# Optimization experiments

Hardware: AMD Instinct MI355X
Metric: run time of the kernel (lower is better)

## Reference

```python
import jax, jax.numpy as jnp
import numpy as np

EMB = 1024
HEADS = 16
DH = EMB // HEADS
EPS = 1e-5


def setup_inputs() -> dict:
    key = jax.random.key(0)
    ks = jax.random.split(key, 8)
    s = 0.02
    return {
        "x": jax.random.normal(ks[0], (4, 2048, EMB), dtype=jnp.float32),
        "Wq": jax.random.normal(ks[1], (EMB, EMB), dtype=jnp.float32) * s,
        "Wk": jax.random.normal(ks[2], (EMB, EMB), dtype=jnp.float32) * s,
        "Wv": jax.random.normal(ks[3], (EMB, EMB), dtype=jnp.float32) * s,
        "Wo": jax.random.normal(ks[4], (EMB, EMB), dtype=jnp.float32) * s,
        "bo": jnp.zeros((EMB,), dtype=jnp.float32),
        "W1": jax.random.normal(ks[5], (EMB, 4 * EMB), dtype=jnp.float32) * s,
        "b1": jnp.zeros((4 * EMB,), dtype=jnp.float32),
        "W2": jax.random.normal(ks[6], (4 * EMB, EMB), dtype=jnp.float32) * s,
        "b2": jnp.zeros((EMB,), dtype=jnp.float32),
        "g1": jnp.ones((EMB,), dtype=jnp.float32),
        "beta1": jnp.zeros((EMB,), dtype=jnp.float32),
        "g2": jnp.ones((EMB,), dtype=jnp.float32),
        "beta2": jnp.zeros((EMB,), dtype=jnp.float32),
    }


def _layernorm(x, scale, bias):
    mean = jnp.mean(x, axis=-1, keepdims=True)
    var = jnp.mean((x - mean) ** 2, axis=-1, keepdims=True)  # unbiased=False
    return scale * ((x - mean) / jnp.sqrt(var + EPS)) + bias


def _attention(x, Wq, Wk, Wv, Wo, bo):
    B, S, _ = x.shape
    q = (x @ Wq).reshape(B, S, HEADS, DH).transpose(0, 2, 1, 3)  # b h s d
    k = (x @ Wk).reshape(B, S, HEADS, DH).transpose(0, 2, 1, 3)
    v = (x @ Wv).reshape(B, S, HEADS, DH).transpose(0, 2, 1, 3)
    scores = jnp.einsum("bhqd,bhkd->bhqk", q, k)
    causal = jnp.tril(jnp.ones((S, S), dtype=bool))
    scores = jnp.where(causal, scores, -jnp.inf)
    w = jax.nn.softmax(scores / jnp.sqrt(jnp.float32(DH)), axis=-1)
    ctx = jnp.einsum("bhqk,bhkd->bhqd", w, v).transpose(0, 2, 1, 3).reshape(B, S, HEADS * DH)
    return ctx @ Wo + bo


def reference(x, Wq, Wk, Wv, Wo, bo, W1, b1, W2, b2, g1, beta1, g2, beta2):
    # pre-LN attention + residual
    h = x + _attention(_layernorm(x, g1, beta1), Wq, Wk, Wv, Wo, bo)
    # pre-LN FFN (exact GELU, as torch nn.GELU default) + residual
    y = _layernorm(h, g2, beta2)
    y = jax.nn.gelu(y @ W1 + b1, approximate=False) @ W2 + b2
    return h + y
```

## Files before the change

### kernel.cpp

```cpp
#include <hip/hip_runtime.h>
#include <hip/hip_bf16.h>

#define EMB 1024
#define SEQ 2048
#define BATCH 4
#define TOK (BATCH*SEQ)
#define NH 16
#define DH 64
#define FF 4096

typedef unsigned short u16;
typedef __bf16 bf16x8 __attribute__((ext_vector_type(8)));
typedef float f32x4 __attribute__((ext_vector_type(4)));

union frag_u { uint4 u4; bf16x8 bf; u16 us[8]; };

__device__ __forceinline__ u16 f2bf(float f) {
  union { float f; unsigned u; } a; a.f = f;
  unsigned r = a.u + 0x7fffu + ((a.u >> 16) & 1u);
  return (u16)(r >> 16);
}
__device__ __forceinline__ float bf2f(u16 u) {
  union { unsigned u; float f; } a; a.u = ((unsigned)u) << 16; return a.f;
}
__device__ __forceinline__ unsigned cvt_pk_bf16(float lo, float hi) {
  unsigned r;
  asm("v_cvt_pk_bf16_f32 %0, %1, %2" : "=v"(r) : "v"(lo), "v"(hi));
  return r;
}
__device__ __forceinline__ float exp2_hw(float x) {
  float r;
  asm("v_exp_f32 %0, %1" : "=v"(r) : "v"(x));
  return r;
}

__device__ __forceinline__ void glds16(const void* g, void* l) {
  __builtin_amdgcn_global_load_lds((const __attribute__((address_space(1))) void*)g,
                                   (__attribute__((address_space(3))) void*)l, 16, 0, 0);
}

__device__ __forceinline__ float gelu_fast(float u) {
  float u2 = u * u;
  float c = fmaf(u2, 0.0356774081f, 0.7978845608f);
  float e = __expf(2.f * u * c);
  return u * e * __builtin_amdgcn_rcpf(e + 1.f);
}

__device__ __forceinline__ void cvt_t_body(const float* __restrict__ src,
                                           u16* __restrict__ dst,
                                           int N, int ldk, int bx, int by) {
  __shared__ float tile[32][33];
  int c0 = bx * 32, r0 = by * 32;
  int tc = threadIdx.x & 31, tr = threadIdx.x >> 5;
  #pragma unroll
  for (int p = 0; p < 4; p++)
    tile[tr + p * 8][tc] = src[(size_t)(r0 + tr + p * 8) * N + c0 + tc];
  __syncthreads();
  #pragma unroll
  for (int p = 0; p < 4; p++)
    dst[(size_t)(c0 + tr + p * 8) * ldk + r0 + tc] = f2bf(tile[tc][tr + p * 8]);
}

__global__ __launch_bounds__(256) void prep_kernel(const float* Wq, const float* Wk,
                                                   const float* Wv, const float* Wo,
                                                   const float* W1, const float* W2,
                                                   u16* wqkv_t, u16* wo_t,
                                                   u16* w1_t, u16* w2_t) {
  int id = blockIdx.x;
  if (id < 4096) {
    const float* s = (id < 1024) ? Wq : (id < 2048) ? Wk : (id < 3072) ? Wv : Wo;
    u16* d = (id < 1024) ? wqkv_t : (id < 2048) ? wqkv_t + 1024 * 1024
           : (id < 3072) ? wqkv_t + 2 * 1024 * 1024 : wo_t;
    int local = id & 1023;
    cvt_t_body(s, d, 1024, 1024, local & 31, local >> 5);
  } else if (id < 8192) {
    int local = id - 4096;
    cvt_t_body(W1, w1_t, 4096, 1024, local & 127, local >> 7);
  } else {
    int local = id - 8192;
    cvt_t_body(W2, w2_t, 1024, 4096, local & 31, local >> 5);
  }
}

template <int IN_BF16>
__global__ __launch_bounds__(256) void ln_kernel(const void* __restrict__ xv,
                                                 const float* __restrict__ g,
                                                 const float* __restrict__ be,
                                                 u16* __restrict__ out) {
  int wave = threadIdx.x >> 6, lane = threadIdx.x & 63;
  int row = blockIdx.x * 4 + wave;
  float v[16];
  float s = 0.f;
  if (IN_BF16) {
    const u16* xr = (const u16*)xv + (size_t)row * EMB;
    #pragma unroll
    for (int i = 0; i < 4; i++) {
      ushort4 u = *(const ushort4*)(xr + i * 256 + lane * 4);
      v[i * 4 + 0] = bf2f(u.x); v[i * 4 + 1] = bf2f(u.y);
      v[i * 4 + 2] = bf2f(u.z); v[i * 4 + 3] = bf2f(u.w);
      s += v[i * 4] + v[i * 4 + 1] + v[i * 4 + 2] + v[i * 4 + 3];
    }
  } else {
    const float* xr = (const float*)xv + (size_t)row * EMB;
    #pragma unroll
    for (int i = 0; i < 4; i++) {
      float4 u = *(const float4*)(xr + i * 256 + lane * 4);
      v[i * 4 + 0] = u.x; v[i * 4 + 1] = u.y; v[i * 4 + 2] = u.z; v[i * 4 + 3] = u.w;
      s += u.x + u.y + u.z + u.w;
    }
  }
  #pragma unroll
  for (int m = 1; m < 64; m <<= 1) s += __shfl_xor(s, m, 64);
  float mean = s * (1.f / EMB);
  float vs = 0.f;
  #pragma unroll
  for (int i = 0; i < 16; i++) { float dx = v[i] - mean; vs += dx * dx; }
  #pragma unroll
  for (int m = 1; m < 64; m <<= 1) vs += __shfl_xor(vs, m, 64);
  float inv = rsqrtf(vs * (1.f / EMB) + 1e-5f);
  u16* orow = out + (size_t)row * EMB;
  #pragma unroll
  for (int i = 0; i < 4; i++) {
    int c = i * 256 + lane * 4;
    float4 gv = *(const float4*)(g + c);
    float4 bv = *(const float4*)(be + c);
    ushort4 o;
    o.x = f2bf(gv.x * (v[i * 4 + 0] - mean) * inv + bv.x);
    o.y = f2bf(gv.y * (v[i * 4 + 1] - mean) * inv + bv.y);
    o.z = f2bf(gv.z * (v[i * 4 + 2] - mean) * inv + bv.z);
    o.w = f2bf(gv.w * (v[i * 4 + 3] - mean) * inv + bv.w);
    *(ushort4*)(orow + c) = o;
  }
}

template <int MODE>
__global__ __launch_bounds__(512) void gemm256(const u16* __restrict__ A,
                                               const u16* __restrict__ Bt,
                                               const float* __restrict__ bias,
                                               void* __restrict__ outp,
                                               int N, int K) {
  __shared__ __align__(16) u16 As[256 * 64];
  __shared__ __align__(16) u16 Bs[128 * 64];
  const int t = threadIdx.x;
  const int w = t >> 6, lane = t & 63;
  const int l15 = lane & 15, quad = lane >> 4;
  const int wr = w >> 1, wc = w & 1;

  const int gx = gridDim.x;
  const int nwg = gx * gridDim.y;
  const int id0 = blockIdx.y * gx + blockIdx.x;
  const int nid = (id0 & 7) * (nwg >> 3) + (id0 >> 3);
  const int rowBase = (nid / gx) * 256, colBase = (nid % gx) * 128;

  const int sr = lane >> 3;
  const int sc = ((lane & 7) ^ sr) * 8;
  const u16* gA = A + (size_t)(rowBase + w * 8 + sr) * K + sc;
  const u16* gB = Bt + (size_t)(colBase + w * 8 + sr) * K + sc;
  u16* lA = As + w * 8 * 64;
  u16* lB = Bs + w * 8 * 64;

  const int swz0 = (quad ^ (l15 & 7)) * 8;
  const int swz1 = ((quad + 4) ^ (l15 & 7)) * 8;

  f32x4 zero = {0.f, 0.f, 0.f, 0.f};
  f32x4 acc[4][4];
  #pragma unroll
  for (int i = 0; i < 4; i++)
    #pragma unroll
    for (int j = 0; j < 4; j++) acc[i][j] = zero;

  for (int k0 = 0; k0 < K; k0 += 64) {
    __syncthreads();
    #pragma unroll
    for (int j = 0; j < 4; j++)
      glds16(gA + (size_t)(j * 64) * K + k0, lA + j * 64 * 64);
    #pragma unroll
    for (int j = 0; j < 2; j++)
      glds16(gB + (size_t)(j * 64) * K + k0, lB + j * 64 * 64);
    __syncthreads();
    #pragma unroll
    for (int kk = 0; kk < 2; kk++) {
      const int so = kk ? swz1 : swz0;
      frag_u a4[4], b4[4];
      #pragma unroll
      for (int mi = 0; mi < 4; mi++)
        a4[mi].u4 = *(const uint4*)(As + (wr * 64 + mi * 16 + l15) * 64 + so);
      #pragma unroll
      for (int ni = 0; ni < 4; ni++)
        b4[ni].u4 = *(const uint4*)(Bs + (wc * 64 + ni * 16 + l15) * 64 + so);
      #pragma unroll
      for (int mi = 0; mi < 4; mi++)
        #pragma unroll
        for (int ni = 0; ni < 4; ni++)
          acc[mi][ni] = __builtin_amdgcn_mfma_f32_16x16x32_bf16(a4[mi].bf, b4[ni].bf, acc[mi][ni], 0, 0, 0);
    }
  }

  #pragma unroll
  for (int mi = 0; mi < 4; mi++) {
    #pragma unroll
    for (int ni = 0; ni < 4; ni++) {
      int col = colBase + wc * 64 + ni * 16 + l15;
      int row0 = rowBase + wr * 64 + mi * 16 + quad * 4;
      if (MODE == 1) {
        int mat = col >> 10, cc = col & 1023;
        int hh = cc >> 6, d = cc & 63;
        int b = row0 >> 11, s0 = row0 & 2047;
        if (mat == 2) {
          uint2 pk;
          pk.x = (unsigned)f2bf(acc[mi][ni][0]) | ((unsigned)f2bf(acc[mi][ni][1]) << 16);
          pk.y = (unsigned)f2bf(acc[mi][ni][2]) | ((unsigned)f2bf(acc[mi][ni][3]) << 16);
          *(uint2*)((u16*)outp + 2 * (size_t)TOK * EMB +
                    ((size_t)((b * NH + hh) * DH + d)) * SEQ + s0) = pk;
        } else {
          const float m = (mat == 0) ? 0.1803368801f : 1.f;
          #pragma unroll
          for (int r = 0; r < 4; r++)
            ((u16*)outp)[(size_t)mat * (TOK * EMB) +
                         (((size_t)(b * NH + hh) * SEQ + s0 + r) << 6) + d] = f2bf(acc[mi][ni][r] * m);
        }
      } else {
        #pragma unroll
        for (int r = 0; r < 4; r++) {
          float vv = gelu_fast(acc[mi][ni][r] + bias[col]);
          ((u16*)outp)[(size_t)(row0 + r) * N + col] = f2bf(vv);
        }
      }
    }
  }
}

template <int MODE>
__global__ __launch_bounds__(256) void gemm128(const u16* __restrict__ A,
                                               const u16* __restrict__ Bt,
                                               const float* __restrict__ bias,
                                               const void* __restrict__ resid,
                                               void* __restrict__ outp,
                                               int N, int K) {
  __shared__ __align__(16) u16 As[2][128 * 64];
  __shared__ __align__(16) u16 Bs[2][128 * 64];
  const int t = threadIdx.x;
  const int w = t >> 6, lane = t & 63;
  const int l15 = lane & 15, quad = lane >> 4;
  const int wr = w >> 1, wc = w & 1;

  const int gx = gridDim.x;
  const int nwg = gx * gridDim.y;
  const int id0 = blockIdx.y * gx + blockIdx.x;
  const int nid = (id0 & 7) * (nwg >> 3) + (id0 >> 3);
  const int rowBase = (nid / gx) * 128, colBase = (nid % gx) * 128;

  const int sr = lane >> 3;
  const int sc = ((lane & 7) ^ sr) * 8;
  const u16* gA = A + (size_t)(rowBase + w * 8 + sr) * K + sc;
  const u16* gB = Bt + (size_t)(colBase + w * 8 + sr) * K + sc;
  const int ldsOff = (w * 8) * 64;

  const int swz0 = (quad ^ (l15 & 7)) * 8;
  const int swz1 = ((quad + 4) ^ (l15 & 7)) * 8;

  f32x4 zero = {0.f, 0.f, 0.f, 0.f};
  f32x4 acc[4][4];
  #pragma unroll
  for (int i = 0; i < 4; i++)
    #pragma unroll
    for (int j = 0; j < 4; j++) acc[i][j] = zero;

  const int nt = K >> 6;
  #pragma unroll
  for (int j = 0; j < 4; j++) {
    glds16(gA + (size_t)(j * 32) * K, As[0] + ldsOff + j * 32 * 64);
    glds16(gB + (size_t)(j * 32) * K, Bs[0] + ldsOff + j * 32 * 64);
  }
  #pragma unroll
  for (int j = 0; j < 4; j++) {
    glds16(gA + (size_t)(j * 32) * K + 64, As[1] + ldsOff + j * 32 * 64);
    glds16(gB + (size_t)(j * 32) * K + 64, Bs[1] + ldsOff + j * 32 * 64);
  }

  for (int tt = 0; tt < nt; tt++) {
    const int cur = tt & 1;
    if (tt + 1 < nt) asm volatile("s_waitcnt vmcnt(8)" ::: "memory");
    else             asm volatile("s_waitcnt vmcnt(0)" ::: "memory");
    __builtin_amdgcn_sched_barrier(0);
    __builtin_amdgcn_s_barrier();

    const u16* as = As[cur];
    const u16* bs = Bs[cur];
    #pragma unroll
    for (int kk = 0; kk < 2; kk++) {
      const int so = kk ? swz1 : swz0;
      frag_u a4[4], b4[4];
      #pragma unroll
      for (int mi = 0; mi < 4; mi++)
        a4[mi].u4 = *(const uint4*)(as + (wr * 64 + mi * 16 + l15) * 64 + so);
      #pragma unroll
      for (int ni = 0; ni < 4; ni++)
        b4[ni].u4 = *(const uint4*)(bs + (wc * 64 + ni * 16 + l15) * 64 + so);
      #pragma unroll
      for (int mi = 0; mi < 4; mi++)
        #pragma unroll
        for (int ni = 0; ni < 4; ni++)
          acc[mi][ni] = __builtin_amdgcn_mfma_f32_16x16x32_bf16(a4[mi].bf, b4[ni].bf, acc[mi][ni], 0, 0, 0);
    }
    asm volatile("s_waitcnt lgkmcnt(0)" ::: "memory");
    __builtin_amdgcn_sched_barrier(0);
    __builtin_amdgcn_s_barrier();

    if (tt + 2 < nt) {
      const int k0 = (tt + 2) << 6;
      #pragma unroll
      for (int j = 0; j < 4; j++) {
        glds16(gA + (size_t)(j * 32) * K + k0, As[cur] + ldsOff + j * 32 * 64);
        glds16(gB + (size_t)(j * 32) * K + k0, Bs[cur] + ldsOff + j * 32 * 64);
      }
    }
  }

  #pragma unroll
  for (int mi = 0; mi < 4; mi++) {
    #pragma unroll
    for (int ni = 0; ni < 4; ni++) {
      int col = colBase + wc * 64 + ni * 16 + l15;
      int row0 = rowBase + wr * 64 + mi * 16 + quad * 4;
      #pragma unroll
      for (int r = 0; r < 4; r++) {
        int row = row0 + r;
        float vv = acc[mi][ni][r] + bias[col];
        if (MODE == 3) {
          vv += ((const float*)resid)[(size_t)row * N + col];
          ((u16*)outp)[(size_t)row * N + col] = f2bf(vv);
        } else {
          vv += bf2f(((const u16*)resid)[(size_t)row * N + col]);
          ((float*)outp)[(size_t)row * N + col] = vv;
        }
      }
    }
  }
}

__global__ __launch_bounds__(256) void attn_kernel(const u16* __restrict__ q,
                                                   const u16* __restrict__ k,
                                                   const u16* __restrict__ vt,
                                                   u16* __restrict__ ctx) {
  __shared__ __align__(16) u16 Ks[64 * 64];
  __shared__ __align__(16) u16 Vs[64 * 64];
  __shared__ __align__(16) u16 Ps[128 * 64];
  __shared__ float Ls[128];
  const int t = threadIdx.x;
  const int w = t >> 6, lane = t & 63;
  const int l15 = lane & 15, quad = lane >> 4;
  const int bh = blockIdx.x;
  const int qt = 15 - (int)blockIdx.y;
  const size_t base = (size_t)bh * SEQ * DH;
  const int bq = bh >> 4, hh = bh & 15;
  const int qBase = qt * 128;
  const int ktEnd = 2 * qt + 1;
  const int l7 = l15 & 7;

  const int r0 = w * 16 + (lane >> 3);
  const int scg = lane & 7;
  const int swzs = (scg ^ (r0 & 7)) * 8;
  const u16* gK = k + base + (size_t)r0 * DH + scg * 8;
  const u16* gV = vt + base + (size_t)r0 * SEQ + scg * 8;
  u16* sK0 = Ks + r0 * 64 + swzs;
  u16* sK1 = Ks + (r0 + 8) * 64 + swzs;
  u16* sV0 = Vs + r0 * 64 + swzs;
  u16* sV1 = Vs + (r0 + 8) * 64 + swzs;

  frag_u qf[2][2];
  #pragma unroll
  for (int ni = 0; ni < 2; ni++)
    #pragma unroll
    for (int ks = 0; ks < 2; ks++)
      qf[ni][ks].u4 = *(const uint4*)(q + base +
          (size_t)(qBase + w * 32 + ni * 16 + l15) * DH + ks * 32 + quad * 8);

  f32x4 zero = {0.f, 0.f, 0.f, 0.f};
  f32x4 oacc[2][4];
  #pragma unroll
  for (int mi = 0; mi < 2; mi++)
    #pragma unroll
    for (int n0 = 0; n0 < 4; n0++) oacc[mi][n0] = zero;
  float l0 = 0.f, l1 = 0.f;

  uint4 rK0 = *(const uint4*)(gK);
  uint4 rK1 = *(const uint4*)(gK + 8 * DH);
  uint4 rV0 = *(const uint4*)(gV);
  uint4 rV1 = *(const uint4*)(gV + (size_t)8 * SEQ);

  for (int kt = 0; kt <= ktEnd; kt++) {
    __syncthreads();
    *(uint4*)sK0 = rK0; *(uint4*)sK1 = rK1;
    *(uint4*)sV0 = rV0; *(uint4*)sV1 = rV1;
    __syncthreads();
    if (kt < ktEnd) {
      const int no = (kt + 1) * 64;
      rK0 = *(const uint4*)(gK + (size_t)no * DH);
      rK1 = *(const uint4*)(gK + (size_t)(no + 8) * DH);
      rV0 = *(const uint4*)(gV + no);
      rV1 = *(const uint4*)(gV + (size_t)8 * SEQ + no);
    }
    const int rel = kt - 2 * qt;
    if (rel == 1 && w < 2) continue;

    frag_u kf[4][2];
    #pragma unroll
    for (int mi = 0; mi < 4; mi++)
      #pragma unroll
      for (int ks = 0; ks < 2; ks++)
        kf[mi][ks].u4 = *(const uint4*)(Ks + (mi * 16 + l15) * 64 + (((ks * 4 + quad) ^ l7) * 8));
    f32x4 st[4][2];
    #pragma unroll
    for (int mi = 0; mi < 4; mi++)
      #pragma unroll
      for (int ni = 0; ni < 2; ni++) st[mi][ni] = zero;
    __builtin_amdgcn_s_setprio(1);
    #pragma unroll
    for (int ks = 0; ks < 2; ks++)
      #pragma unroll
      for (int mi = 0; mi < 4; mi++)
        #pragma unroll
        for (int ni = 0; ni < 2; ni++)
          st[mi][ni] = __builtin_amdgcn_mfma_f32_16x16x32_bf16(kf[mi][ks].bf, qf[ni][ks].bf, st[mi][ni], 0, 0, 0);
    __builtin_amdgcn_s_setprio(0);

    const bool doMask = (rel == 0 && w < 2) || (rel == 1);
    #pragma unroll
    for (int ni = 0; ni < 2; ni++) {
      const int qrow = qBase + w * 32 + ni * 16 + l15;
      float sum = 0.f;
      u16* prow = Ps + (w * 32 + ni * 16 + l15) * 64;
      #pragma unroll
      for (int mi = 0; mi < 4; mi++) {
        float p[4];
        if (doMask) {
          #pragma unroll
          for (int r = 0; r < 4; r++) {
            p[r] = exp2_hw(st[mi][ni][r]);
            if ((kt * 64 + mi * 16 + quad * 4 + r) > qrow) p[r] = 0.f;
            sum += p[r];
          }
        } else {
          #pragma unroll
          for (int r = 0; r < 4; r++) {
            p[r] = exp2_hw(st[mi][ni][r]);
            sum += p[r];
          }
        }
        uint2 pk;
        pk.x = cvt_pk_bf16(p[0], p[1]);
        pk.y = cvt_pk_bf16(p[2], p[3]);
        *(uint2*)(prow + (((mi * 2 + (quad >> 1)) ^ l7) * 8) + (quad & 1) * 4) = pk;
      }
      sum += __shfl_xor(sum, 16, 64);
      sum += __shfl_xor(sum, 32, 64);
      if (ni == 0) l0 += sum; else l1 += sum;
    }

    frag_u pa[2][2];
    #pragma unroll
    for (int mi = 0; mi < 2; mi++)
      #pragma unroll
      for (int ks = 0; ks < 2; ks++)
        pa[mi][ks].u4 = *(const uint4*)(Ps + (w * 32 + mi * 16 + l15) * 64 + (((ks * 4 + quad) ^ l7) * 8));
    __builtin_amdgcn_s_setprio(1);
    #pragma unroll
    for (int ks = 0; ks < 2; ks++)
      #pragma unroll
      for (int n0 = 0; n0 < 4; n0++) {
        frag_u b;
        b.u4 = *(const uint4*)(Vs + (n0 * 16 + l15) * 64 + (((ks * 4 + quad) ^ l7) * 8));
        #pragma unroll
        for (int mi = 0; mi < 2; mi++)
          oacc[mi][n0] = __builtin_amdgcn_mfma_f32_16x16x32_bf16(pa[mi][ks].bf, b.bf, oacc[mi][n0], 0, 0, 0);
      }
    __builtin_amdgcn_s_setprio(0);
  }

  if (quad == 0) {
    Ls[w * 32 + l15] = l0;
    Ls[w * 32 + 16 + l15] = l1;
  }
  #pragma unroll
  for (int mi = 0; mi < 2; mi++) {
    float il[4];
    #pragma unroll
    for (int r = 0; r < 4; r++) il[r] = 1.f / Ls[w * 32 + mi * 16 + quad * 4 + r];
    #pragma unroll
    for (int n0 = 0; n0 < 4; n0++) {
      int s = qBase + w * 32 + mi * 16 + quad * 4;
      int col = hh * 64 + n0 * 16 + l15;
      #pragma unroll
      for (int r = 0; r < 4; r++)
        ctx[((size_t)(bq * SEQ + s + r)) * EMB + col] = f2bf(oacc[mi][n0][r] * il[r]);
    }
  }
}

extern "C" void kernel_launch(void* const* d_in, const int* in_sizes, int n_in,
                              void* d_out, int out_size, void* d_ws, size_t ws_size,
                              hipStream_t stream) {
  const float* x  = (const float*)d_in[0];
  const float* Wq = (const float*)d_in[1];
  const float* Wk = (const float*)d_in[2];
  const float* Wv = (const float*)d_in[3];
  const float* Wo = (const float*)d_in[4];
  const float* bo = (const float*)d_in[5];
  const float* W1 = (const float*)d_in[6];
  const float* b1 = (const float*)d_in[7];
  const float* W2 = (const float*)d_in[8];
  const float* b2 = (const float*)d_in[9];
  const float* g1  = (const float*)d_in[10];
  const float* be1 = (const float*)d_in[11];
  const float* g2  = (const float*)d_in[12];
  const float* be2 = (const float*)d_in[13];
  float* out = (float*)d_out;
  char* ws = (char*)d_ws;
  const size_t MB = 1u << 20;

  u16* wqkv_t = (u16*)(ws + 0 * MB);
  u16* wo_t   = (u16*)(ws + 6 * MB);
  u16* w1_t   = (u16*)(ws + 8 * MB);
  u16* w2_t   = (u16*)(ws + 16 * MB);
  u16* hbuf   = (u16*)(ws + 24 * MB);
  u16* r1 = (u16*)(ws + 56 * MB);
  u16* qb = (u16*)(ws + 72 * MB);
  u16* f1 = (u16*)(ws + 72 * MB);

  prep_kernel<<<12288, 256, 0, stream>>>(Wq, Wk, Wv, Wo, W1, W2,
                                         wqkv_t, wo_t, w1_t, w2_t);

  ln_kernel<0><<<2048, 256, 0, stream>>>(x, g1, be1, r1);

  gemm256<1><<<dim3(24, 32), 512, 0, stream>>>(r1, wqkv_t, nullptr, qb, 3072, 1024);

  attn_kernel<<<dim3(64, 16), 256, 0, stream>>>(qb, qb + (size_t)TOK * EMB,
                                                qb + 2 * (size_t)TOK * EMB, r1);

  gemm128<3><<<dim3(8, 64), 256, 0, stream>>>(r1, wo_t, bo, x, hbuf, 1024, 1024);

  ln_kernel<1><<<2048, 256, 0, stream>>>(hbuf, g2, be2, r1);

  gemm256<2><<<dim3(32, 32), 512, 0, stream>>>(r1, w1_t, b1, f1, 4096, 1024);

  gemm128<4><<<dim3(8, 64), 256, 0, stream>>>(f1, w2_t, b2, hbuf, out, 1024, 4096);
}
```

Measured before the change: 441.9 us.

## Fuse LN1 into weight prep, widen transpose tiles, add MFMA priority, reorder attention tiles

The weight transpose-convert now uses 64x64 tiles with float4 loads and 16-byte bf16 stores in place of 32x32 tiles with scalar accesses. The first LayerNorm is folded into the prep kernel as extra blocks, which removes one launch. The two GEMMs raise wave priority around their MFMA loops with s_setprio, and the attention kernel maps blockIdx.y to an interleaved order of causal query tiles to balance load. Risks are extra LDS per block for the larger tile and higher register pressure in the combined prep kernel.

```diff
diff --git a/kernel.cpp b/kernel.cpp
--- a/kernel.cpp
+++ b/kernel.cpp
@@ -46,49 +46,38 @@
   return u * e * __builtin_amdgcn_rcpf(e + 1.f);
 }
 
-__device__ __forceinline__ void cvt_t_body(const float* __restrict__ src,
-                                           u16* __restrict__ dst,
-                                           int N, int ldk, int bx, int by) {
-  __shared__ float tile[32][33];
-  int c0 = bx * 32, r0 = by * 32;
-  int tc = threadIdx.x & 31, tr = threadIdx.x >> 5;
-  #pragma unroll
-  for (int p = 0; p < 4; p++)
-    tile[tr + p * 8][tc] = src[(size_t)(r0 + tr + p * 8) * N + c0 + tc];
+__device__ __forceinline__ void cvt_t64(const float* __restrict__ src,
+                                        u16* __restrict__ dst,
+                                        int N, int ldk, int bx, int by) {
+  __shared__ float tile[64][65];
+  const int t = threadIdx.x;
+  const int c0 = bx * 64, r0 = by * 64;
+  const int tr = t >> 4, tc = t & 15;
+  #pragma unroll
+  for (int p = 0; p < 4; p++) {
+    float4 v = *(const float4*)(src + (size_t)(r0 + p * 16 + tr) * N + c0 + tc * 4);
+    tile[p * 16 + tr][tc * 4 + 0] = v.x;
+    tile[p * 16 + tr][tc * 4 + 1] = v.y;
+    tile[p * 16 + tr][tc * 4 + 2] = v.z;
+    tile[p * 16 + tr][tc * 4 + 3] = v.w;
+  }
   __syncthreads();
-  #pragma unroll
-  for (int p = 0; p < 4; p++)
-    dst[(size_t)(c0 + tr + p * 8) * ldk + r0 + tc] = f2bf(tile[tc][tr + p * 8]);
-}
-
-__global__ __launch_bounds__(256) void prep_kernel(const float* Wq, const float* Wk,
-                                                   const float* Wv, const float* Wo,
-                                                   const float* W1, const float* W2,
-                                                   u16* wqkv_t, u16* wo_t,
-                                                   u16* w1_t, u16* w2_t) {
-  int id = blockIdx.x;
-  if (id < 4096) {
-    const float* s = (id < 1024) ? Wq : (id < 2048) ? Wk : (id < 3072) ? Wv : Wo;
-    u16* d = (id < 1024) ? wqkv_t : (id < 2048) ? wqkv_t + 1024 * 1024
-           : (id < 3072) ? wqkv_t + 2 * 1024 * 1024 : wo_t;
-    int local = id & 1023;
-    cvt_t_body(s, d, 1024, 1024, local & 31, local >> 5);
-  } else if (id < 8192) {
-    int local = id - 4096;
-    cvt_t_body(W1, w1_t, 4096, 1024, local & 127, local >> 7);
-  } else {
-    int local = id - 8192;
-    cvt_t_body(W2, w2_t, 1024, 4096, local & 31, local >> 5);
-  }
+  const int cr = t >> 2, ch = t & 3;
+  union { u16 us[16]; uint4 u4[2]; } o;
+  #pragma unroll
+  for (int j = 0; j < 16; j++) o.us[j] = f2bf(tile[ch * 16 + j][cr]);
+  u16* drow = dst + (size_t)(c0 + cr) * ldk + r0 + ch * 16;
+  *(uint4*)(drow) = o.u4[0];
+  *(uint4*)(drow + 8) = o.u4[1];
 }
 
 template <int IN_BF16>
-__global__ __launch_bounds__(256) void ln_kernel(const void* __restrict__ xv,
-                                                 const float* __restrict__ g,
-                                                 const float* __restrict__ be,
-                                                 u16* __restrict__ out) {
+__device__ __forceinline__ void ln_body(const void* __restrict__ xv,
+                                        const float* __restrict__ g,
+                                        const float* __restrict__ be,
+                                        u16* __restrict__ out, int blk) {
   int wave = threadIdx.x >> 6, lane = threadIdx.x & 63;
-  int row = blockIdx.x * 4 + wave;
+  int row = blk * 4 + wave;
   float v[16];
   float s = 0.f;
   if (IN_BF16) {
@@ -130,6 +119,39 @@
     o.z = f2bf(gv.z * (v[i * 4 + 2] - mean) * inv + bv.z);
     o.w = f2bf(gv.w * (v[i * 4 + 3] - mean) * inv + bv.w);
     *(ushort4*)(orow + c) = o;
+  }
+}
+
+template <int IN_BF16>
+__global__ __launch_bounds__(256) void ln_kernel(const void* __restrict__ xv,
+                                                 const float* __restrict__ g,
+                                                 const float* __restrict__ be,
+                                                 u16* __restrict__ out) {
+  ln_body<IN_BF16>(xv, g, be, out, blockIdx.x);
+}
+
+__global__ __launch_bounds__(256) void prep_kernel(const float* Wq, const float* Wk,
+                                                   const float* Wv, const float* Wo,
+                                                   const float* W1, const float* W2,
+                                                   u16* wqkv_t, u16* wo_t,
+                                                   u16* w1_t, u16* w2_t,
+                                                   const float* x, const float* g1,
+                                                   const float* be1, u16* xn1) {
+  int id = blockIdx.x;
+  if (id < 1024) {
+    int mat = id >> 8, local = id & 255;
+    const float* s = (mat == 0) ? Wq : (mat == 1) ? Wk : (mat == 2) ? Wv : Wo;
+    u16* d = (mat == 0) ? wqkv_t : (mat == 1) ? wqkv_t + 1024 * 1024
+           : (mat == 2) ? wqkv_t + 2 * 1024 * 1024 : wo_t;
+    cvt_t64(s, d, 1024, 1024, local & 15, local >> 4);
+  } else if (id < 2048) {
+    int local = id - 1024;
+    cvt_t64(W1, w1_t, 4096, 1024, local & 63, local >> 6);
+  } else if (id < 3072) {
+    int local = id - 2048;
+    cvt_t64(W2, w2_t, 1024, 4096, local & 15, local >> 4);
+  } else {
+    ln_body<0>(x, g1, be1, xn1, id - 3072);
   }
 }
 
@@ -188,11 +210,13 @@
       #pragma unroll
       for (int ni = 0; ni < 4; ni++)
         b4[ni].u4 = *(const uint4*)(Bs + (wc * 64 + ni * 16 + l15) * 64 + so);
+      __builtin_amdgcn_s_setprio(1);
       #pragma unroll
       for (int mi = 0; mi < 4; mi++)
         #pragma unroll
         for (int ni = 0; ni < 4; ni++)
           acc[mi][ni] = __builtin_amdgcn_mfma_f32_16x16x32_bf16(a4[mi].bf, b4[ni].bf, acc[mi][ni], 0, 0, 0);
+      __builtin_amdgcn_s_setprio(0);
     }
   }
 
@@ -297,11 +321,13 @@
       #pragma unroll
       for (int ni = 0; ni < 4; ni++)
         b4[ni].u4 = *(const uint4*)(bs + (wc * 64 + ni * 16 + l15) * 64 + so);
+      __builtin_amdgcn_s_setprio(1);
       #pragma unroll
       for (int mi = 0; mi < 4; mi++)
         #pragma unroll
         for (int ni = 0; ni < 4; ni++)
           acc[mi][ni] = __builtin_amdgcn_mfma_f32_16x16x32_bf16(a4[mi].bf, b4[ni].bf, acc[mi][ni], 0, 0, 0);
+      __builtin_amdgcn_s_setprio(0);
     }
     asm volatile("s_waitcnt lgkmcnt(0)" ::: "memory");
     __builtin_amdgcn_sched_barrier(0);
@@ -351,7 +377,9 @@
   const int w = t >> 6, lane = t & 63;
   const int l15 = lane & 15, quad = lane >> 4;
   const int bh = blockIdx.x;
-  const int qt = 15 - (int)blockIdx.y;
+  const int y = (int)blockIdx.y;
+  const int qt = (y < 4) ? (15 - 2 * y) : (y < 8) ? (22 - 2 * y)
+               : (y < 12) ? (2 * y - 15) : (2 * y - 24);
   const size_t base = (size_t)bh * SEQ * DH;
   const int bq = bh >> 4, hh = bh & 15;
   const int qBase = qt * 128;
@@ -528,10 +556,9 @@
   u16* qb = (u16*)(ws + 72 * MB);
   u16* f1 = (u16*)(ws + 72 * MB);
 
-  prep_kernel<<<12288, 256, 0, stream>>>(Wq, Wk, Wv, Wo, W1, W2,
-                                         wqkv_t, wo_t, w1_t, w2_t);
-
-  ln_kernel<0><<<2048, 256, 0, stream>>>(x, g1, be1, r1);
+  prep_kernel<<<5120, 256, 0, stream>>>(Wq, Wk, Wv, Wo, W1, W2,
+                                        wqkv_t, wo_t, w1_t, w2_t,
+                                        x, g1, be1, r1);
 
   gemm256<1><<<dim3(24, 32), 512, 0, stream>>>(r1, wqkv_t, nullptr, qb, 3072, 1024);
 
```

Result: slower. 458.9 us (+3.8%).
